# Kernel tuning notes

Measured on AMD Instinct MI355X. Metric: run time of the kernel, lower is better.

## Reference

```python
import jax, jax.numpy as jnp
import numpy as np

N = 100000      # nodes
E = 1600000     # edges
G = 1000        # graphs in the batch
D_IN, D_H, D_OUT = 128, 128, 64


def setup_inputs() -> dict:
    key = jax.random.key(0)
    ks = jax.random.split(key, 8)
    x = jax.random.normal(ks[0], (N, D_IN), jnp.float32)
    edge_index = jax.random.randint(ks[1], (2, E), 0, N, dtype=jnp.int32)
    batch = jnp.sort(jax.random.randint(ks[2], (N,), 0, G, dtype=jnp.int32))
    s_in = 1.0 / np.sqrt(D_IN)
    s_h = 1.0 / np.sqrt(D_H)
    return {
        "x": x,
        "edge_index": edge_index,
        "batch": batch,
        "W_emb": jax.random.normal(ks[3], (D_IN, D_H), jnp.float32) * s_in,
        "b_emb": jnp.zeros((D_H,), jnp.float32),
        "W1": jax.random.normal(ks[4], (D_H, D_H), jnp.float32) * s_h,
        "b1": jnp.zeros((D_H,), jnp.float32),
        "W2": jax.random.normal(ks[5], (D_H, D_H), jnp.float32) * s_h,
        "b2": jnp.zeros((D_H,), jnp.float32),
        "W3": jax.random.normal(ks[6], (D_H, D_OUT), jnp.float32) * s_h,
        "b3": jnp.zeros((D_OUT,), jnp.float32),
    }


def reference(x, edge_index, batch, W_emb, b_emb, W1, b1, W2, b2, W3, b3):
    # Eval mode: dropout is identity.
    n = x.shape[0]
    src, dst = edge_index[0], edge_index[1]
    # GCN symmetric normalization with self-loops (Kipf & Welling).
    deg = jax.ops.segment_sum(jnp.ones(src.shape[0], x.dtype), dst, num_segments=n) + 1.0
    dis = jax.lax.rsqrt(deg)                 # deg^{-1/2}, [N]
    edge_norm = dis[src] * dis[dst]          # [E]
    self_norm = dis * dis                    # self-loop weight = 1/deg, [N]

    def gcn_conv(h, W, b):
        h = h @ W                                         # [N, d_out]
        agg = jax.ops.segment_sum(h[src] * edge_norm[:, None], dst, num_segments=n)
        return agg + h * self_norm[:, None] + b

    h = x @ W_emb + b_emb
    h = jax.nn.relu(gcn_conv(h, W1, b1))
    h = jax.nn.relu(gcn_conv(h, W2, b2))
    h = gcn_conv(h, W3, b3)
    # global_add_pool over graph ids
    return jax.ops.segment_sum(h, batch, num_segments=G)
```

## Files before the change

kernel.cpp:

```cpp
#include <hip/hip_runtime.h>
#include <hip/hip_bf16.h>

#define NN 100000
#define NE 1600000
#define NG 1000
#define SMAX 48

typedef unsigned short u16;
typedef unsigned int u32;
typedef u16 u16x8 __attribute__((ext_vector_type(8)));
typedef u32 u32x4 __attribute__((ext_vector_type(4)));
typedef float f32x4 __attribute__((ext_vector_type(4)));
typedef __attribute__((ext_vector_type(8))) short s16x8;
typedef __attribute__((ext_vector_type(4))) float facc4;

__device__ __forceinline__ float bf2f(u16 u) {
    union { u32 i; float f; } c; c.i = ((u32)u) << 16; return c.f;
}
__device__ __forceinline__ u16 f2bf(float f) {
    __hip_bfloat16 h = __float2bfloat16(f);
    union { __hip_bfloat16 h; u16 u; } c; c.h = h; return c.u;
}
__device__ __forceinline__ int ntload(const int* p) { return __builtin_nontemporal_load(p); }

__global__ __launch_bounds__(256) void detect_kernel(const u32* __restrict__ xr, int* __restrict__ flag) {
    __shared__ int cnt[256];
    int c = 0;
    for (int i = threadIdx.x; i < 4096; i += 256) {
        u32 e = (xr[i] >> 7) & 0xFFu;
        if (e >= 110u && e <= 135u) c++;
    }
    cnt[threadIdx.x] = c;
    __syncthreads();
    for (int o = 128; o > 0; o >>= 1) {
        if (threadIdx.x < o) cnt[threadIdx.x] += cnt[threadIdx.x + o];
        __syncthreads();
    }
    if (threadIdx.x == 0) flag[0] = (cnt[0] > 2048) ? 1 : 0;
}

#define MEGA_NB 12726
__global__ __launch_bounds__(256) void mega_prep(
    const void* __restrict__ x, const int* __restrict__ flag, u16* __restrict__ xb,
    const void* __restrict__ Wemb, const void* __restrict__ W1, const void* __restrict__ W2,
    const void* __restrict__ W3, u16* __restrict__ wembT, u16* __restrict__ w1T,
    u16* __restrict__ w2T, u16* __restrict__ w3T,
    const void* __restrict__ bemb, const void* __restrict__ b1, const void* __restrict__ b2,
    const void* __restrict__ b3, float* __restrict__ bembF, float* __restrict__ b1F,
    float* __restrict__ b2F, float* __restrict__ b3F,
    const int* __restrict__ ei, int* __restrict__ counts)
{
    int b = blockIdx.x, tid = threadIdx.x;
    int fl = flag[0];
    if (b < 6250) {
        if (fl) return;
        int c = b * 256 + tid;
        f32x4 a = reinterpret_cast<const f32x4*>(x)[c * 2];
        f32x4 d = reinterpret_cast<const f32x4*>(x)[c * 2 + 1];
        u16x8 o;
        #pragma unroll
        for (int j = 0; j < 4; ++j) { o[j] = f2bf(a[j]); o[4 + j] = f2bf(d[j]); }
        reinterpret_cast<u16x8*>(xb)[c] = o;
    } else if (b < 6474) {
        int o = (b - 6250) * 256 + tid;
        const void* src; u16* dst; int M; int ol;
        if (o < 16384)      { src = Wemb; dst = wembT; M = 128; ol = o; }
        else if (o < 32768) { src = W1;   dst = w1T;   M = 128; ol = o - 16384; }
        else if (o < 49152) { src = W2;   dst = w2T;   M = 128; ol = o - 32768; }
        else                { src = W3;   dst = w3T;   M = 64;  ol = o - 49152; }
        int n = ol >> 7, k = ol & 127;
        u16 v = fl ? reinterpret_cast<const u16*>(src)[k * M + n]
                   : f2bf(reinterpret_cast<const float*>(src)[k * M + n]);
        dst[ol] = v;
    } else if (b < 6476) {
        int i = (b - 6474) * 256 + tid;
        if (i >= 448) return;
        const void* src; float* dst; int il;
        if (i < 128)      { src = bemb; dst = bembF; il = i; }
        else if (i < 256) { src = b1;   dst = b1F;   il = i - 128; }
        else if (i < 384) { src = b2;   dst = b2F;   il = i - 256; }
        else              { src = b3;   dst = b3F;   il = i - 384; }
        dst[il] = fl ? bf2f(reinterpret_cast<const u16*>(src)[il])
                     : reinterpret_cast<const float*>(src)[il];
    } else {
        int e = (b - 6476) * 256 + tid;
        if (e < NE) atomicAdd(&counts[ei[NE + e]], 1);
    }
}

__global__ __launch_bounds__(256) void wfuse_kernel(const u16* __restrict__ w1T, const u16* __restrict__ wembT,
                                                    const float* __restrict__ bembF,
                                                    u16* __restrict__ WfT, float* __restrict__ bfW) {
    int b = blockIdx.x;
    if (b < 64) {
        int o = b * 256 + threadIdx.x;
        int n = o >> 7, k = o & 127;
        float acc = 0.f;
        #pragma unroll 4
        for (int j = 0; j < 128; ++j)
            acc += bf2f(w1T[n * 128 + j]) * bf2f(wembT[j * 128 + k]);
        WfT[o] = f2bf(acc);
    } else {
        int n = threadIdx.x;
        if (n < 128) {
            float acc = 0.f;
            for (int j = 0; j < 128; ++j)
                acc += bembF[j] * bf2f(w1T[n * 128 + j]);
            bfW[n] = acc;
        }
    }
}

__global__ __launch_bounds__(256) void scan1_kernel(const int* __restrict__ counts, int* __restrict__ offs,
                                                    int* __restrict__ bsums, float* __restrict__ dis,
                                                    int* __restrict__ cursor) {
    __shared__ int sums[256];
    int tid = threadIdx.x;
    int base = blockIdx.x * 2048 + tid * 8;
    int local[8];
    int s = 0;
    #pragma unroll
    for (int i = 0; i < 8; ++i) {
        int v = 0;
        if (base + i < NN) {
            v = counts[base + i];
            dis[base + i] = rsqrtf((float)v + 1.0f);
            cursor[base + i] = 0;
        }
        local[i] = s; s += v;
    }
    sums[tid] = s;
    __syncthreads();
    for (int o = 1; o < 256; o <<= 1) {
        int v = (tid >= o) ? sums[tid - o] : 0;
        __syncthreads();
        sums[tid] += v;
        __syncthreads();
    }
    int excl = sums[tid] - s;
    #pragma unroll
    for (int i = 0; i < 8; ++i)
        if (base + i < NN) offs[base + i] = excl + local[i];
    if (tid == 255) bsums[blockIdx.x] = sums[255];
}

__global__ __launch_bounds__(256) void scan3_kernel(int* __restrict__ offs, const int* __restrict__ bsums) {
    __shared__ int addv;
    int i = blockIdx.x * 256 + threadIdx.x;
    int bucket = blockIdx.x >> 3;
    if (threadIdx.x == 0) {
        int s = 0;
        for (int k = 0; k < bucket; ++k) s += bsums[k];
        addv = s;
    }
    __syncthreads();
    if (i < NN) offs[i] += addv;
}

#define MEGA2_SCAT 6250
__global__ __launch_bounds__(256, 5) void mega2_kernel(
    const u16* __restrict__ xb, const u16* __restrict__ xraw, const int* __restrict__ flag,
    const u16* __restrict__ WfT, const float* __restrict__ bfW, u16* __restrict__ Hout,
    const int* __restrict__ ei, const int* __restrict__ offs, int* __restrict__ cursor,
    int* __restrict__ srcs)
{
    int b = blockIdx.x, tid = threadIdx.x;
    if (b < MEGA2_SCAT) {
        int e = b * 256 + tid;
        if (e < NE) {
            int s = ei[e], d = ei[NE + e];
            int pos = offs[d] + atomicAdd(&cursor[d], 1);
            srcs[pos] = s;
        }
    } else {
        const u16* A = flag[0] ? xraw : xb;
        int gb = b - MEGA2_SCAT;
        int wv = tid >> 6, lane = tid & 63;
        int m = lane & 15, quad = lane >> 4;
        int r0 = gb * 64 + wv * 16;
        int ar = r0 + m; if (ar >= NN) ar = NN - 1;
        facc4 acc[8];
        #pragma unroll
        for (int t = 0; t < 8; ++t) acc[t] = (facc4){0.f, 0.f, 0.f, 0.f};
        const u16* arow = A + (size_t)ar * 128 + quad * 8;
        #pragma unroll
        for (int k0 = 0; k0 < 128; k0 += 32) {
            s16x8 a = *reinterpret_cast<const s16x8*>(arow + k0);
            #pragma unroll
            for (int t = 0; t < 8; ++t) {
                s16x8 bfr = *reinterpret_cast<const s16x8*>(WfT + (t * 16 + m) * 128 + k0 + quad * 8);
                acc[t] = __builtin_amdgcn_mfma_f32_16x16x32_bf16(a, bfr, acc[t], 0, 0, 0);
            }
        }
        #pragma unroll
        for (int t = 0; t < 8; ++t) {
            int col = t * 16 + m;
            float bv = bfW[col];
            #pragma unroll
            for (int r = 0; r < 4; ++r) {
                int orow = r0 + quad * 4 + r;
                if (orow < NN)
                    Hout[(size_t)orow * 128 + col] = f2bf(acc[t][r] + bv);
            }
        }
    }
}

template <int MOUT>
__global__ __launch_bounds__(256) void fused_agg_gemm(const u16* __restrict__ T, const int* __restrict__ offs,
                                                      const int* __restrict__ counts, const float* __restrict__ dis,
                                                      const int* __restrict__ srcs, const float* __restrict__ aggbias,
                                                      const u16* __restrict__ Wt, u16* __restrict__ Hout) {
    constexpr int LDW = 136;
    __shared__ u16 sW[MOUT * LDW];
    __shared__ u16 sA[64 * LDW];
    int tid = threadIdx.x;
    for (int c = tid; c < MOUT * 16; c += 256) {
        int n = c >> 4, kc = (c & 15) << 3;
        *reinterpret_cast<u16x8*>(sW + n * LDW + kc) = reinterpret_cast<const u16x8*>(Wt)[c];
    }

    int lane = tid & 15, grp = tid >> 4;
    const u32x4* T4 = reinterpret_cast<const u32x4*>(T);
    for (int i = 0; i < 4; ++i) {
        int nl = grp * 4 + i;
        int n = blockIdx.x * 64 + nl;
        bool valid = n < NN;
        int nc = valid ? n : NN - 1;
        float di = dis[nc];
        float sn = di * di;
        u32x4 ts = T4[(size_t)nc * 16 + lane];
        float acc[8];
        #pragma unroll
        for (int q = 0; q < 4; ++q) {
            acc[2 * q]     = bf2f((u16)(ts[q] & 0xffffu)) * sn + aggbias[lane * 8 + 2 * q];
            acc[2 * q + 1] = bf2f((u16)(ts[q] >> 16))     * sn + aggbias[lane * 8 + 2 * q + 1];
        }
        int st = offs[nc], cnt = valid ? counts[nc] : 0;
        int j = 0;
        for (; j + 4 <= cnt; j += 4) {
            int e0 = ntload(srcs + st + j);
            int e1 = ntload(srcs + st + j + 1);
            int e2 = ntload(srcs + st + j + 2);
            int e3 = ntload(srcs + st + j + 3);
            float w0 = dis[e0] * di, w1 = dis[e1] * di, w2 = dis[e2] * di, w3 = dis[e3] * di;
            u32x4 g0 = T4[(size_t)e0 * 16 + lane];
            u32x4 g1 = T4[(size_t)e1 * 16 + lane];
            u32x4 g2 = T4[(size_t)e2 * 16 + lane];
            u32x4 g3 = T4[(size_t)e3 * 16 + lane];
            #pragma unroll
            for (int q = 0; q < 4; ++q) {
                acc[2 * q]     += bf2f((u16)(g0[q] & 0xffffu)) * w0;
                acc[2 * q + 1] += bf2f((u16)(g0[q] >> 16))     * w0;
                acc[2 * q]     += bf2f((u16)(g1[q] & 0xffffu)) * w1;
                acc[2 * q + 1] += bf2f((u16)(g1[q] >> 16))     * w1;
                acc[2 * q]     += bf2f((u16)(g2[q] & 0xffffu)) * w2;
                acc[2 * q + 1] += bf2f((u16)(g2[q] >> 16))     * w2;
                acc[2 * q]     += bf2f((u16)(g3[q] & 0xffffu)) * w3;
                acc[2 * q + 1] += bf2f((u16)(g3[q] >> 16))     * w3;
            }
        }
        for (; j < cnt; ++j) {
            int e = ntload(srcs + st + j);
            float w = dis[e] * di;
            u32x4 g = T4[(size_t)e * 16 + lane];
            #pragma unroll
            for (int q = 0; q < 4; ++q) {
                acc[2 * q]     += bf2f((u16)(g[q] & 0xffffu)) * w;
                acc[2 * q + 1] += bf2f((u16)(g[q] >> 16))     * w;
            }
        }
        u16x8 pk;
        #pragma unroll
        for (int q = 0; q < 4; ++q) {
            pk[2 * q]     = f2bf(fmaxf(acc[2 * q], 0.0f));
            pk[2 * q + 1] = f2bf(fmaxf(acc[2 * q + 1], 0.0f));
        }
        *reinterpret_cast<u16x8*>(sA + nl * LDW + lane * 8) = pk;
    }
    __syncthreads();

    int wv = tid >> 6, l64 = tid & 63;
    int m = l64 & 15, quad = l64 >> 4;
    int r0 = blockIdx.x * 64 + wv * 16;
    constexpr int NT = MOUT / 16;
    facc4 gacc[NT];
    #pragma unroll
    for (int t = 0; t < NT; ++t) gacc[t] = (facc4){0.f, 0.f, 0.f, 0.f};
    #pragma unroll
    for (int k0 = 0; k0 < 128; k0 += 32) {
        s16x8 a = *reinterpret_cast<const s16x8*>(sA + (wv * 16 + m) * LDW + k0 + quad * 8);
        #pragma unroll
        for (int t = 0; t < NT; ++t) {
            s16x8 bfr = *reinterpret_cast<const s16x8*>(sW + (t * 16 + m) * LDW + k0 + quad * 8);
            gacc[t] = __builtin_amdgcn_mfma_f32_16x16x32_bf16(a, bfr, gacc[t], 0, 0, 0);
        }
    }
    #pragma unroll
    for (int t = 0; t < NT; ++t) {
        int col = t * 16 + m;
        #pragma unroll
        for (int r = 0; r < 4; ++r) {
            int orow = r0 + quad * 4 + r;
            if (orow < NN)
                Hout[(size_t)orow * MOUT + col] = f2bf(gacc[t][r]);
        }
    }
}

__global__ __launch_bounds__(256) void agg_pool_kernel(const u16* __restrict__ T, const int* __restrict__ offs,
                                                       const int* __restrict__ counts, const float* __restrict__ dis,
                                                       const int* __restrict__ srcs, const float* __restrict__ bias,
                                                       const int* __restrict__ batch, float* __restrict__ outF) {
    __shared__ float accG[SMAX * 64];
    __shared__ int sg0;
    int tid = threadIdx.x;
    for (int i = tid; i < SMAX * 64; i += 256) accG[i] = 0.0f;
    if (tid == 0) sg0 = batch[blockIdx.x * 32];
    __syncthreads();
    int g0 = sg0;
    int lane = tid & 7;
    int n = blockIdx.x * 32 + (tid >> 3);

    const u32x4* T4 = reinterpret_cast<const u32x4*>(T);
    float di = dis[n];
    float sn = di * di;
    u32x4 ts = T4[(size_t)n * 8 + lane];
    float acc[8];
    #pragma unroll
    for (int q = 0; q < 4; ++q) {
        acc[2 * q]     = bf2f((u16)(ts[q] & 0xffffu)) * sn + bias[lane * 8 + 2 * q];
        acc[2 * q + 1] = bf2f((u16)(ts[q] >> 16))     * sn + bias[lane * 8 + 2 * q + 1];
    }
    int st = offs[n], cnt = counts[n];
    int j = 0;
    for (; j + 4 <= cnt; j += 4) {
        int e0 = ntload(srcs + st + j);
        int e1 = ntload(srcs + st + j + 1);
        int e2 = ntload(srcs + st + j + 2);
        int e3 = ntload(srcs + st + j + 3);
        float w0 = dis[e0] * di, w1 = dis[e1] * di, w2 = dis[e2] * di, w3 = dis[e3] * di;
        u32x4 g0v = T4[(size_t)e0 * 8 + lane];
        u32x4 g1v = T4[(size_t)e1 * 8 + lane];
        u32x4 g2v = T4[(size_t)e2 * 8 + lane];
        u32x4 g3v = T4[(size_t)e3 * 8 + lane];
        #pragma unroll
        for (int q = 0; q < 4; ++q) {
            acc[2 * q]     += bf2f((u16)(g0v[q] & 0xffffu)) * w0;
            acc[2 * q + 1] += bf2f((u16)(g0v[q] >> 16))     * w0;
            acc[2 * q]     += bf2f((u16)(g1v[q] & 0xffffu)) * w1;
            acc[2 * q + 1] += bf2f((u16)(g1v[q] >> 16))     * w1;
            acc[2 * q]     += bf2f((u16)(g2v[q] & 0xffffu)) * w2;
            acc[2 * q + 1] += bf2f((u16)(g2v[q] >> 16))     * w2;
            acc[2 * q]     += bf2f((u16)(g3v[q] & 0xffffu)) * w3;
            acc[2 * q + 1] += bf2f((u16)(g3v[q] >> 16))     * w3;
        }
    }
    for (; j < cnt; ++j) {
        int e = ntload(srcs + st + j);
        float w = dis[e] * di;
        u32x4 g = T4[(size_t)e * 8 + lane];
        #pragma unroll
        for (int q = 0; q < 4; ++q) {
            acc[2 * q]     += bf2f((u16)(g[q] & 0xffffu)) * w;
            acc[2 * q + 1] += bf2f((u16)(g[q] >> 16))     * w;
        }
    }

    int s = batch[n] - g0;
    if (s >= 0 && s < SMAX) {
        #pragma unroll
        for (int q = 0; q < 8; ++q)
            atomicAdd(&accG[s * 64 + lane * 8 + q], acc[q]);
    } else {
        #pragma unroll
        for (int q = 0; q < 8; ++q)
            atomicAdd(&outF[(size_t)(g0 + s) * 64 + lane * 8 + q], acc[q]);
    }
    __syncthreads();
    int gend = batch[blockIdx.x * 32 + 31];
    int span = gend - g0 + 1;
    if (span > SMAX) span = SMAX;
    for (int i = tid; i < span * 64; i += 256)
        atomicAdd(&outF[(size_t)g0 * 64 + i], accG[i]);
}

__global__ __launch_bounds__(256) void out_cvt_kernel(const float* __restrict__ outF, void* __restrict__ out,
                                                      const int* __restrict__ flag) {
    int i = blockIdx.x * 256 + threadIdx.x;
    if (i < NG * 64) {
        float v = outF[i];
        if (flag[0]) reinterpret_cast<u16*>(out)[i] = f2bf(v);
        else         reinterpret_cast<float*>(out)[i] = v;
    }
}

extern "C" void kernel_launch(void* const* d_in, const int* in_sizes, int n_in,
                              void* d_out, int out_size, void* d_ws, size_t ws_size,
                              hipStream_t stream) {
    const void* x     = d_in[0];
    const int* ei     = (const int*)d_in[1];
    const int* batch  = (const int*)d_in[2];
    const void* W_emb = d_in[3];
    const void* b_emb = d_in[4];
    const void* W1    = d_in[5];
    const void* b1    = d_in[6];
    const void* W2    = d_in[7];
    const void* b2    = d_in[8];
    const void* W3    = d_in[9];
    const void* b3    = d_in[10];

    char* p = (char*)d_ws;
    auto alloc = [&](size_t bytes) { void* r = p; p += (bytes + 255) & ~(size_t)255; return r; };
    int*   flag   = (int*)alloc(256);
    int*   counts = (int*)alloc(NN * 4);
    int*   cursor = (int*)alloc(NN * 4);
    int*   offs   = (int*)alloc(NN * 4);
    float* dis    = (float*)alloc(NN * 4);
    int*   bsums  = (int*)alloc(256 * 4);
    int*   srcs   = (int*)alloc((size_t)NE * 4);
    u16*   wembT  = (u16*)alloc(128 * 128 * 2);
    u16*   w1T    = (u16*)alloc(128 * 128 * 2);
    u16*   w2T    = (u16*)alloc(128 * 128 * 2);
    u16*   w3T    = (u16*)alloc(64 * 128 * 2);
    u16*   WfT    = (u16*)alloc(128 * 128 * 2);
    float* bembF  = (float*)alloc(128 * 4);
    float* b1F    = (float*)alloc(128 * 4);
    float* b2F    = (float*)alloc(128 * 4);
    float* b3F    = (float*)alloc(64 * 4);
    float* bfW    = (float*)alloc(128 * 4);
    float* outF   = (float*)alloc((size_t)NG * 64 * 4);
    u16*   hA     = (u16*)alloc((size_t)(NN + 64) * 128 * 2);
    u16*   hB     = (u16*)alloc((size_t)(NN + 64) * 128 * 2);

    hipMemsetAsync(counts, 0, NN * 4, stream);
    hipMemsetAsync(outF, 0, (size_t)NG * 64 * 4, stream);

    const int SB = (NN + 2047) / 2048;
    const int NB = (NN + 255) / 256;
    const int GB = (NN + 63) / 64;

    detect_kernel<<<1, 256, 0, stream>>>((const u32*)x, flag);
    mega_prep<<<MEGA_NB, 256, 0, stream>>>(x, flag, hB, W_emb, W1, W2, W3, wembT, w1T, w2T, w3T,
                                           b_emb, b1, b2, b3, bembF, b1F, b2F, b3F, ei, counts);
    wfuse_kernel<<<65, 256, 0, stream>>>(w1T, wembT, bembF, WfT, bfW);
    scan1_kernel<<<SB, 256, 0, stream>>>(counts, offs, bsums, dis, cursor);
    scan3_kernel<<<NB, 256, 0, stream>>>(offs, bsums);

    mega2_kernel<<<MEGA2_SCAT + GB, 256, 0, stream>>>(hB, (const u16*)x, flag, WfT, bfW, hA,
                                                      ei, offs, cursor, srcs);
    fused_agg_gemm<128><<<GB, 256, 0, stream>>>(hA, offs, counts, dis, srcs, b1F, w2T, hB);
    fused_agg_gemm<64><<<GB, 256, 0, stream>>>(hB, offs, counts, dis, srcs, b2F, w3T, hA);
    agg_pool_kernel<<<NN / 32, 256, 0, stream>>>(hA, offs, counts, dis, srcs, b3F, batch, outF);
    out_cvt_kernel<<<(NG * 64 + 255) / 256, 256, 0, stream>>>(outF, d_out, flag);
}
```

Baseline: 582.0 us.

## Split scatter/GEMM megakernel, stage GEMM weights in LDS, unroll gathers by eight

Splits the combined edge-scatter and embedding-GEMM kernel into two separate launches. The GEMM now stages the fused weight matrix in padded shared memory instead of reading it from global memory for every MFMA. The neighbour-gather loops in the two aggregation kernels get an 8-wide unrolled path so more independent loads are in flight. In exchange, the scatter and GEMM no longer run concurrently inside one launch, and the wider unroll raises register pressure.

Result: slower. 596.1 us (+2.4%).

```diff
diff --git a/kernel.cpp b/kernel.cpp
--- a/kernel.cpp
+++ b/kernel.cpp
@@ -157,51 +157,53 @@
     if (i < NN) offs[i] += addv;
 }
 
-#define MEGA2_SCAT 6250
-__global__ __launch_bounds__(256, 5) void mega2_kernel(
-    const u16* __restrict__ xb, const u16* __restrict__ xraw, const int* __restrict__ flag,
-    const u16* __restrict__ WfT, const float* __restrict__ bfW, u16* __restrict__ Hout,
-    const int* __restrict__ ei, const int* __restrict__ offs, int* __restrict__ cursor,
-    int* __restrict__ srcs)
-{
-    int b = blockIdx.x, tid = threadIdx.x;
-    if (b < MEGA2_SCAT) {
-        int e = b * 256 + tid;
-        if (e < NE) {
-            int s = ei[e], d = ei[NE + e];
-            int pos = offs[d] + atomicAdd(&cursor[d], 1);
-            srcs[pos] = s;
-        }
-    } else {
-        const u16* A = flag[0] ? xraw : xb;
-        int gb = b - MEGA2_SCAT;
-        int wv = tid >> 6, lane = tid & 63;
-        int m = lane & 15, quad = lane >> 4;
-        int r0 = gb * 64 + wv * 16;
-        int ar = r0 + m; if (ar >= NN) ar = NN - 1;
-        facc4 acc[8];
-        #pragma unroll
-        for (int t = 0; t < 8; ++t) acc[t] = (facc4){0.f, 0.f, 0.f, 0.f};
-        const u16* arow = A + (size_t)ar * 128 + quad * 8;
-        #pragma unroll
-        for (int k0 = 0; k0 < 128; k0 += 32) {
-            s16x8 a = *reinterpret_cast<const s16x8*>(arow + k0);
-            #pragma unroll
-            for (int t = 0; t < 8; ++t) {
-                s16x8 bfr = *reinterpret_cast<const s16x8*>(WfT + (t * 16 + m) * 128 + k0 + quad * 8);
-                acc[t] = __builtin_amdgcn_mfma_f32_16x16x32_bf16(a, bfr, acc[t], 0, 0, 0);
-            }
-        }
+__global__ __launch_bounds__(256) void scatter_kernel(const int* __restrict__ ei, const int* __restrict__ offs,
+                                                      int* __restrict__ cursor, int* __restrict__ srcs) {
+    int e = blockIdx.x * 256 + threadIdx.x;
+    if (e < NE) {
+        int s = ei[e], d = ei[NE + e];
+        int pos = offs[d] + atomicAdd(&cursor[d], 1);
+        srcs[pos] = s;
+    }
+}
+
+__global__ __launch_bounds__(256) void gemm_emb(const u16* __restrict__ xb, const u16* __restrict__ xraw,
+                                                const int* __restrict__ flag, const u16* __restrict__ WfT,
+                                                const float* __restrict__ bfW, u16* __restrict__ Hout) {
+    __shared__ u16 sW[128 * 136];
+    int tid = threadIdx.x;
+    const u16* A = flag[0] ? xraw : xb;
+    for (int c = tid; c < 128 * 16; c += 256) {
+        int n = c >> 4, kc = (c & 15) << 3;
+        *reinterpret_cast<u16x8*>(sW + n * 136 + kc) = reinterpret_cast<const u16x8*>(WfT)[c];
+    }
+    __syncthreads();
+    int wv = tid >> 6, lane = tid & 63;
+    int m = lane & 15, quad = lane >> 4;
+    int r0 = blockIdx.x * 64 + wv * 16;
+    int ar = r0 + m; if (ar >= NN) ar = NN - 1;
+    facc4 acc[8];
+    #pragma unroll
+    for (int t = 0; t < 8; ++t) acc[t] = (facc4){0.f, 0.f, 0.f, 0.f};
+    const u16* arow = A + (size_t)ar * 128 + quad * 8;
+    #pragma unroll
+    for (int k0 = 0; k0 < 128; k0 += 32) {
+        s16x8 a = *reinterpret_cast<const s16x8*>(arow + k0);
         #pragma unroll
         for (int t = 0; t < 8; ++t) {
-            int col = t * 16 + m;
-            float bv = bfW[col];
-            #pragma unroll
-            for (int r = 0; r < 4; ++r) {
-                int orow = r0 + quad * 4 + r;
-                if (orow < NN)
-                    Hout[(size_t)orow * 128 + col] = f2bf(acc[t][r] + bv);
-            }
+            s16x8 bfr = *reinterpret_cast<const s16x8*>(sW + (t * 16 + m) * 136 + k0 + quad * 8);
+            acc[t] = __builtin_amdgcn_mfma_f32_16x16x32_bf16(a, bfr, acc[t], 0, 0, 0);
+        }
+    }
+    #pragma unroll
+    for (int t = 0; t < 8; ++t) {
+        int col = t * 16 + m;
+        float bv = bfW[col];
+        #pragma unroll
+        for (int r = 0; r < 4; ++r) {
+            int orow = r0 + quad * 4 + r;
+            if (orow < NN)
+                Hout[(size_t)orow * 128 + col] = f2bf(acc[t][r] + bv);
         }
     }
 }
@@ -238,27 +240,37 @@
         }
         int st = offs[nc], cnt = valid ? counts[nc] : 0;
         int j = 0;
+        for (; j + 8 <= cnt; j += 8) {
+            int e[8]; float w[8]; u32x4 g[8];
+            #pragma unroll
+            for (int u = 0; u < 8; ++u) e[u] = ntload(srcs + st + j + u);
+            #pragma unroll
+            for (int u = 0; u < 8; ++u) w[u] = dis[e[u]] * di;
+            #pragma unroll
+            for (int u = 0; u < 8; ++u) g[u] = T4[(size_t)e[u] * 16 + lane];
+            #pragma unroll
+            for (int u = 0; u < 8; ++u)
+                #pragma unroll
+                for (int q = 0; q < 4; ++q) {
+                    acc[2 * q]     += bf2f((u16)(g[u][q] & 0xffffu)) * w[u];
+                    acc[2 * q + 1] += bf2f((u16)(g[u][q] >> 16))     * w[u];
+                }
+        }
         for (; j + 4 <= cnt; j += 4) {
-            int e0 = ntload(srcs + st + j);
-            int e1 = ntload(srcs + st + j + 1);
-            int e2 = ntload(srcs + st + j + 2);
-            int e3 = ntload(srcs + st + j + 3);
-            float w0 = dis[e0] * di, w1 = dis[e1] * di, w2 = dis[e2] * di, w3 = dis[e3] * di;
-            u32x4 g0 = T4[(size_t)e0 * 16 + lane];
-            u32x4 g1 = T4[(size_t)e1 * 16 + lane];
-            u32x4 g2 = T4[(size_t)e2 * 16 + lane];
-            u32x4 g3 = T4[(size_t)e3 * 16 + lane];
-            #pragma unroll
-            for (int q = 0; q < 4; ++q) {
-                acc[2 * q]     += bf2f((u16)(g0[q] & 0xffffu)) * w0;
-                acc[2 * q + 1] += bf2f((u16)(g0[q] >> 16))     * w0;
-                acc[2 * q]     += bf2f((u16)(g1[q] & 0xffffu)) * w1;
-                acc[2 * q + 1] += bf2f((u16)(g1[q] >> 16))     * w1;
-                acc[2 * q]     += bf2f((u16)(g2[q] & 0xffffu)) * w2;
-                acc[2 * q + 1] += bf2f((u16)(g2[q] >> 16))     * w2;
-                acc[2 * q]     += bf2f((u16)(g3[q] & 0xffffu)) * w3;
-                acc[2 * q + 1] += bf2f((u16)(g3[q] >> 16))     * w3;
-            }
+            int e[4]; float w[4]; u32x4 g[4];
+            #pragma unroll
+            for (int u = 0; u < 4; ++u) e[u] = ntload(srcs + st + j + u);
+            #pragma unroll
+            for (int u = 0; u < 4; ++u) w[u] = dis[e[u]] * di;
+            #pragma unroll
+            for (int u = 0; u < 4; ++u) g[u] = T4[(size_t)e[u] * 16 + lane];
+            #pragma unroll
+            for (int u = 0; u < 4; ++u)
+                #pragma unroll
+                for (int q = 0; q < 4; ++q) {
+                    acc[2 * q]     += bf2f((u16)(g[u][q] & 0xffffu)) * w[u];
+                    acc[2 * q + 1] += bf2f((u16)(g[u][q] >> 16))     * w[u];
+                }
         }
         for (; j < cnt; ++j) {
             int e = ntload(srcs + st + j);
@@ -334,27 +346,37 @@
     }
     int st = offs[n], cnt = counts[n];
     int j = 0;
+    for (; j + 8 <= cnt; j += 8) {
+        int e[8]; float w[8]; u32x4 g[8];
+        #pragma unroll
+        for (int u = 0; u < 8; ++u) e[u] = ntload(srcs + st + j + u);
+        #pragma unroll
+        for (int u = 0; u < 8; ++u) w[u] = dis[e[u]] * di;
+        #pragma unroll
+        for (int u = 0; u < 8; ++u) g[u] = T4[(size_t)e[u] * 8 + lane];
+        #pragma unroll
+        for (int u = 0; u < 8; ++u)
+            #pragma unroll
+            for (int q = 0; q < 4; ++q) {
+                acc[2 * q]     += bf2f((u16)(g[u][q] & 0xffffu)) * w[u];
+                acc[2 * q + 1] += bf2f((u16)(g[u][q] >> 16))     * w[u];
+            }
+    }
     for (; j + 4 <= cnt; j += 4) {
-        int e0 = ntload(srcs + st + j);
-        int e1 = ntload(srcs + st + j + 1);
-        int e2 = ntload(srcs + st + j + 2);
-        int e3 = ntload(srcs + st + j + 3);
-        float w0 = dis[e0] * di, w1 = dis[e1] * di, w2 = dis[e2] * di, w3 = dis[e3] * di;
-        u32x4 g0v = T4[(size_t)e0 * 8 + lane];
-        u32x4 g1v = T4[(size_t)e1 * 8 + lane];
-        u32x4 g2v = T4[(size_t)e2 * 8 + lane];
-        u32x4 g3v = T4[(size_t)e3 * 8 + lane];
-        #pragma unroll
-        for (int q = 0; q < 4; ++q) {
-            acc[2 * q]     += bf2f((u16)(g0v[q] & 0xffffu)) * w0;
-            acc[2 * q + 1] += bf2f((u16)(g0v[q] >> 16))     * w0;
-            acc[2 * q]     += bf2f((u16)(g1v[q] & 0xffffu)) * w1;
-            acc[2 * q + 1] += bf2f((u16)(g1v[q] >> 16))     * w1;
-            acc[2 * q]     += bf2f((u16)(g2v[q] & 0xffffu)) * w2;
-            acc[2 * q + 1] += bf2f((u16)(g2v[q] >> 16))     * w2;
-            acc[2 * q]     += bf2f((u16)(g3v[q] & 0xffffu)) * w3;
-            acc[2 * q + 1] += bf2f((u16)(g3v[q] >> 16))     * w3;
-        }
+        int e[4]; float w[4]; u32x4 g[4];
+        #pragma unroll
+        for (int u = 0; u < 4; ++u) e[u] = ntload(srcs + st + j + u);
+        #pragma unroll
+        for (int u = 0; u < 4; ++u) w[u] = dis[e[u]] * di;
+        #pragma unroll
+        for (int u = 0; u < 4; ++u) g[u] = T4[(size_t)e[u] * 8 + lane];
+        #pragma unroll
+        for (int u = 0; u < 4; ++u)
+            #pragma unroll
+            for (int q = 0; q < 4; ++q) {
+                acc[2 * q]     += bf2f((u16)(g[u][q] & 0xffffu)) * w[u];
+                acc[2 * q + 1] += bf2f((u16)(g[u][q] >> 16))     * w[u];
+            }
     }
     for (; j < cnt; ++j) {
         int e = ntload(srcs + st + j);
@@ -439,6 +461,7 @@
     const int SB = (NN + 2047) / 2048;
     const int NB = (NN + 255) / 256;
     const int GB = (NN + 63) / 64;
+    const int EB = (NE + 255) / 256;
 
     detect_kernel<<<1, 256, 0, stream>>>((const u32*)x, flag);
     mega_prep<<<MEGA_NB, 256, 0, stream>>>(x, flag, hB, W_emb, W1, W2, W3, wembT, w1T, w2T, w3T,
@@ -446,9 +469,8 @@
     wfuse_kernel<<<65, 256, 0, stream>>>(w1T, wembT, bembF, WfT, bfW);
     scan1_kernel<<<SB, 256, 0, stream>>>(counts, offs, bsums, dis, cursor);
     scan3_kernel<<<NB, 256, 0, stream>>>(offs, bsums);
-
-    mega2_kernel<<<MEGA2_SCAT + GB, 256, 0, stream>>>(hB, (const u16*)x, flag, WfT, bfW, hA,
-                                                      ei, offs, cursor, srcs);
+    scatter_kernel<<<EB, 256, 0, stream>>>(ei, offs, cursor, srcs);
+    gemm_emb<<<GB, 256, 0, stream>>>(hB, (const u16*)x, flag, WfT, bfW, hA);
     fused_agg_gemm<128><<<GB, 256, 0, stream>>>(hA, offs, counts, dis, srcs, b1F, w2T, hB);
     fused_agg_gemm<64><<<GB, 256, 0, stream>>>(hB, offs, counts, dis, srcs, b2F, w3T, hA);
     agg_pool_kernel<<<NN / 32, 256, 0, stream>>>(hA, offs, counts, dis, srcs, b3F, batch, outF);
```
